# Optimization experiments

Measured on AMD Instinct MI355X. Metric: run time of the kernel, lower is better.

## Reference

```python
import jax, jax.numpy as jnp
import numpy as np

DIM, EMBED, HEADS = 768, 512, 8
HEAD_DIM = EMBED // HEADS


def setup_inputs() -> dict:
    key = jax.random.key(0)
    ks = jax.random.split(key, 11)
    B, S = 4, 2048
    s = 0.02
    return {
        "query": jax.random.normal(ks[0], (B, S, DIM), jnp.float32),
        "key": jax.random.normal(ks[1], (B, S, DIM), jnp.float32),
        "value": jax.random.normal(ks[2], (B, S, DIM), jnp.float32),
        "wq": jax.random.normal(ks[3], (DIM, EMBED), jnp.float32) * s,
        "bq": jnp.zeros((EMBED,), jnp.float32),
        "wk": jax.random.normal(ks[4], (DIM, EMBED), jnp.float32) * s,
        "bk": jnp.zeros((EMBED,), jnp.float32),
        "wv": jax.random.normal(ks[5], (DIM, EMBED), jnp.float32) * s,
        "bv": jnp.zeros((EMBED,), jnp.float32),
        "wo": jax.random.normal(ks[6], (EMBED, DIM), jnp.float32) * s,
        "bo": jnp.zeros((DIM,), jnp.float32),
    }


def reference(query, key, value, wq, bq, wk, bk, wv, bv, wo, bo):
    B, S, _ = query.shape
    # QKV projections -> [B, H, S, Dh]
    def split_heads(x):
        return x.reshape(B, -1, HEADS, HEAD_DIM).transpose(0, 2, 1, 3)
    q = split_heads(query @ wq + bq)
    k = split_heads(key @ wk + bk)
    v = split_heads(value @ wv + bv)
    scores = jnp.einsum("bhqd,bhkd->bhqk", q, k) / jnp.sqrt(jnp.float32(HEAD_DIM))
    p = jax.nn.softmax(scores, axis=-1)
    x = jnp.einsum("bhqk,bhkd->bhqd", p, v)
    x = x.transpose(0, 2, 1, 3).reshape(B, S, EMBED)
    return x @ wo + bo
```

## Files before the change

### kernel.cpp

```cpp
#include <hip/hip_runtime.h>
#include <math.h>

#define NH   8
#define HD   64
#define BS   4
#define SEQL 2048
#define DIMX 768
#define EMB  512
#define MROWS (BS*SEQL)
#define NSPLIT 2
#define KSPAN (SEQL/NSPLIT)

typedef __attribute__((ext_vector_type(4))) float          f32x4;
typedef __attribute__((ext_vector_type(8))) __bf16         bf16x8;
typedef __attribute__((ext_vector_type(8))) unsigned short u16x8;
typedef __attribute__((ext_vector_type(4))) unsigned short u16x4;

union BF8 { u16x8 u; bf16x8 b; };

__device__ __forceinline__ unsigned short f2bf(float x) {
    unsigned int u = __float_as_uint(x);
    u += 0x7FFFu + ((u >> 16) & 1u);
    return (unsigned short)(u >> 16);
}

#if __has_builtin(__builtin_amdgcn_exp2f)
#define EXP2F(x) __builtin_amdgcn_exp2f(x)
#else
#define EXP2F(x) exp2f(x)
#endif

__device__ __forceinline__ bf16x8 ldb8(const unsigned short* p) {
    return *(const bf16x8*)p;
}

__device__ __forceinline__ void gload16(const unsigned short* g, unsigned short* l) {
    __builtin_amdgcn_global_load_lds(
        (const __attribute__((address_space(1))) unsigned int*)(const void*)g,
        (__attribute__((address_space(3))) unsigned int*)(void*)l,
        16, 0, 0);
}

__global__ __launch_bounds__(256)
void transpose_w4(const float* __restrict__ w0, const float* __restrict__ w1,
                  const float* __restrict__ w2, const float* __restrict__ w3,
                  unsigned short* __restrict__ o0, unsigned short* __restrict__ o1,
                  unsigned short* __restrict__ o2, unsigned short* __restrict__ o3)
{
    __shared__ float sm[32][33];
    const int which = blockIdx.y;
    const float* in; unsigned short* out; int R, C;
    if      (which == 0) { in = w0; out = o0; R = DIMX; C = EMB;  }
    else if (which == 1) { in = w1; out = o1; R = DIMX; C = EMB;  }
    else if (which == 2) { in = w2; out = o2; R = DIMX; C = EMB;  }
    else                 { in = w3; out = o3; R = EMB;  C = DIMX; }
    const int nbx = C / 32;
    const int rB = (blockIdx.x / nbx) * 32, cB = (blockIdx.x % nbx) * 32;
    const int row = threadIdx.x >> 3, c4 = (threadIdx.x & 7) * 4;
    f32x4 v = *(const f32x4*)&in[(size_t)(rB + row) * C + cB + c4];
    sm[row][c4 + 0] = v[0]; sm[row][c4 + 1] = v[1];
    sm[row][c4 + 2] = v[2]; sm[row][c4 + 3] = v[3];
    __syncthreads();
    u16x4 o;
    o[0] = f2bf(sm[c4 + 0][row]); o[1] = f2bf(sm[c4 + 1][row]);
    o[2] = f2bf(sm[c4 + 2][row]); o[3] = f2bf(sm[c4 + 3][row]);
    *(u16x4*)&out[(size_t)(cB + row) * R + rB + c4] = o;
}

template<bool DIRECT, int AMODE>
__device__ __forceinline__ void gemm_core(
    const float* __restrict__ A, const float* __restrict__ A2,
    const float* __restrict__ lp0, const float* __restrict__ lp1,
    const unsigned short* __restrict__ Bt,
    int K, int lda, int mBase, int nBase,
    unsigned short* __restrict__ smA, unsigned short* __restrict__ smB,
    f32x4 (&acc)[4][4])
{
    const int tid = threadIdx.x;
    const int lane = tid & 63, w = tid >> 6;
    const int quad = lane >> 4, lanem = lane & 15;
    const int wm = w >> 1, wn = w & 1;
    const int r8 = lane >> 3, ch = lane & 7;
    const int swz = ((ch ^ r8) << 3);

    const f32x4 z4 = {0.f, 0.f, 0.f, 0.f};
    #pragma unroll
    for (int i = 0; i < 4; ++i)
        #pragma unroll
        for (int j = 0; j < 4; ++j) acc[i][j] = z4;

    const int fxor = (lanem & 7);

    for (int k0 = 0; k0 < K; k0 += 64) {
        u16x8 sa[4];
        #pragma unroll
        for (int j = 0; j < 4; ++j) {
            const int m = mBase + (w * 4 + j) * 8 + r8;
            const int kc = k0 + swz;
            if constexpr (AMODE == 1) {
                const float* ap = &A[(size_t)m * lda + kc];
                f32x4 x0 = *(const f32x4*)ap;
                f32x4 x1 = *(const f32x4*)(ap + 4);
                #pragma unroll
                for (int r = 0; r < 4; ++r) { sa[j][r] = f2bf(x0[r]); sa[j][4 + r] = f2bf(x1[r]); }
            } else {
                const int q = m & 2047, bb = m >> 11, hh = kc >> 6, dd = kc & 63;
                const size_t off = ((((size_t)((bb << 3) | hh)) * 2048 + q) << 6) + dd;
                f32x4 a0 = *(const f32x4*)&A [off];
                f32x4 a1 = *(const f32x4*)&A [off + 4];
                f32x4 c0 = *(const f32x4*)&A2[off];
                f32x4 c1 = *(const f32x4*)&A2[off + 4];
                const float rl = 1.f / (lp0[off >> 6] + lp1[off >> 6]);
                #pragma unroll
                for (int r = 0; r < 4; ++r) {
                    sa[j][r]     = f2bf((a0[r] + c0[r]) * rl);
                    sa[j][4 + r] = f2bf((a1[r] + c1[r]) * rl);
                }
            }
        }
        __syncthreads();
        #pragma unroll
        for (int j = 0; j < 4; ++j)
            *(u16x8*)&smA[(w * 4 + j) * 512 + lane * 8] = sa[j];
        #pragma unroll
        for (int j = 0; j < 4; ++j) {
            const int row = (w * 4 + j) * 8 + r8;
            gload16(&Bt[(size_t)(nBase + row) * K + k0 + swz], smB + (w * 4 + j) * 512);
        }
        __syncthreads();
        #pragma unroll
        for (int kk = 0; kk < 64; kk += 32) {
            const int cb = kk >> 3;
            bf16x8 xa[4], wb[4];
            #pragma unroll
            for (int mt = 0; mt < 4; ++mt)
                xa[mt] = ldb8(&smA[(wm * 64 + mt * 16 + lanem) * 64 + (((cb + quad) ^ fxor) << 3)]);
            #pragma unroll
            for (int nt = 0; nt < 4; ++nt)
                wb[nt] = ldb8(&smB[(wn * 64 + nt * 16 + lanem) * 64 + (((cb + quad) ^ fxor) << 3)]);
            if constexpr (DIRECT) {
                #pragma unroll
                for (int mt = 0; mt < 4; ++mt)
                    #pragma unroll
                    for (int nt = 0; nt < 4; ++nt)
                        acc[mt][nt] = __builtin_amdgcn_mfma_f32_16x16x32_bf16(xa[mt], wb[nt], acc[mt][nt], 0, 0, 0);
            } else {
                #pragma unroll
                for (int nt = 0; nt < 4; ++nt)
                    #pragma unroll
                    for (int mt = 0; mt < 4; ++mt)
                        acc[nt][mt] = __builtin_amdgcn_mfma_f32_16x16x32_bf16(wb[nt], xa[mt], acc[nt][mt], 0, 0, 0);
            }
        }
    }
}

__global__ __launch_bounds__(256)
void gemm_qkv(const float* __restrict__ Xq, const float* __restrict__ Xk,
              const float* __restrict__ Xv, const unsigned short* __restrict__ Wt,
              const float* __restrict__ bq, const float* __restrict__ bk,
              const float* __restrict__ bv,
              unsigned short* __restrict__ Qb, unsigned short* __restrict__ Kb,
              unsigned short* __restrict__ Vtb)
{
    __shared__ unsigned short smA[128 * 64];
    __shared__ unsigned short smB[128 * 64];
    const int id = blockIdx.x;
    const int xcd = id & 7, j = id >> 3;
    const int nIdx = j & 3, pr = j >> 2;
    const int p = pr * 8 + xcd;
    const int z = p >> 6;
    const int mBase = (p & 63) * 128, nBase = nIdx * 128;

    const float* A = z == 0 ? Xq : (z == 1 ? Xk : Xv);
    const unsigned short* Bt = Wt + (size_t)z * (EMB * DIMX);
    const float* bias = z == 0 ? bq : (z == 1 ? bk : bv);

    const int tid = threadIdx.x;
    const int lane = tid & 63, w = tid >> 6;
    const int quad = lane >> 4, lanem = lane & 15;
    const int wm = w >> 1, wn = w & 1;

    f32x4 acc[4][4];
    if (z == 2) {
        gemm_core<true, 1>(A, nullptr, nullptr, nullptr, Bt, DIMX, DIMX, mBase, nBase, smA, smB, acc);
        #pragma unroll
        for (int mt = 0; mt < 4; ++mt) {
            const int sg = mBase + wm * 64 + mt * 16 + quad * 4;
            const int b = sg >> 11, s = sg & 2047;
            #pragma unroll
            for (int nt = 0; nt < 4; ++nt) {
                const int de = nBase + wn * 64 + nt * 16 + lanem;
                const float bvv = bias[de];
                const int h = de >> 6, dh = de & 63;
                u16x4 ov;
                #pragma unroll
                for (int r = 0; r < 4; ++r) ov[r] = f2bf(acc[mt][nt][r] + bvv);
                *(u16x4*)&Vtb[((size_t)((b * NH + h) * HD + dh) << 11) + s] = ov;
            }
        }
    } else {
        gemm_core<false, 1>(A, nullptr, nullptr, nullptr, Bt, DIMX, DIMX, mBase, nBase, smA, smB, acc);
        const float os = (z == 0) ? 0.18033688f : 1.0f;
        unsigned short* C = (z == 0) ? Qb : Kb;
        #pragma unroll
        for (int nt = 0; nt < 4; ++nt) {
            const int n0 = nBase + wn * 64 + nt * 16 + quad * 4;
            const f32x4 b4 = *(const f32x4*)&bias[n0];
            #pragma unroll
            for (int mt = 0; mt < 4; ++mt) {
                const int m = mBase + wm * 64 + mt * 16 + lanem;
                u16x4 ov;
                #pragma unroll
                for (int r = 0; r < 4; ++r) ov[r] = f2bf((acc[nt][mt][r] + b4[r]) * os);
                *(u16x4*)&C[(size_t)m * EMB + n0] = ov;
            }
        }
    }
}

__global__ __launch_bounds__(256)
void gemm_out(const float* __restrict__ Opart, const float* __restrict__ lpart,
              const unsigned short* __restrict__ Wot,
              const float* __restrict__ bo, float* __restrict__ out)
{
    __shared__ unsigned short smA[128 * 64];
    __shared__ unsigned short smB[128 * 64];
    const int id = blockIdx.x;
    const int xcd = id & 7, j = id >> 3;
    const int nIdx = j % 6, pr = j / 6;
    const int mBase = (pr * 8 + xcd) * 128, nBase = nIdx * 128;
    const int tid = threadIdx.x;
    const int lane = tid & 63, w = tid >> 6;
    const int quad = lane >> 4, lanem = lane & 15;
    const int wm = w >> 1, wn = w & 1;

    const float* Op1 = Opart + (size_t)32 * SEQL * HD;
    const float* lp1 = lpart + (size_t)32 * SEQL;

    f32x4 acc[4][4];
    gemm_core<false, 2>(Opart, Op1, lpart, lp1, Wot, EMB, EMB, mBase, nBase, smA, smB, acc);
    #pragma unroll
    for (int nt = 0; nt < 4; ++nt) {
        const int n0 = nBase + wn * 64 + nt * 16 + quad * 4;
        const f32x4 b4 = *(const f32x4*)&bo[n0];
        #pragma unroll
        for (int mt = 0; mt < 4; ++mt) {
            const int m = mBase + wm * 64 + mt * 16 + lanem;
            f32x4 ov = acc[nt][mt] + b4;
            *(f32x4*)&out[(size_t)m * DIMX + n0] = ov;
        }
    }
}

__global__ __launch_bounds__(256)
void attn_mfma(const unsigned short* __restrict__ Qb, const unsigned short* __restrict__ Kb,
               const unsigned short* __restrict__ Vt,
               float* __restrict__ Opart, float* __restrict__ lpart)
{
    __shared__ unsigned short smK[64 * 72];
    __shared__ unsigned short smV[64 * 72];
    __shared__ unsigned short smP[4][32 * 72];
    const int id = blockIdx.x;
    const int bh = ((id & 7) << 2) | ((id >> 3) & 3);
    const int rest = id >> 5;
    const int qb = rest & 15, sp = rest >> 4;
    const int b = bh >> 3, h = bh & 7;

    const int tid = threadIdx.x;
    const int w = tid >> 6, lane = tid & 63;
    const int quad = lane >> 4, lanem = lane & 15;

    bf16x8 aq[2][2];
    #pragma unroll
    for (int rg = 0; rg < 2; ++rg) {
        const size_t qrow = (size_t)(b * SEQL + qb * 128 + w * 32 + rg * 16 + lanem) * EMB + h * HD;
        aq[rg][0] = ldb8(&Qb[qrow + quad * 8]);
        aq[rg][1] = ldb8(&Qb[qrow + 32 + quad * 8]);
    }

    const f32x4 z4 = {0.f, 0.f, 0.f, 0.f};
    f32x4 o[4][2];
    f32x4 ls[2] = {z4, z4};
    #pragma unroll
    for (int dt = 0; dt < 4; ++dt)
        #pragma unroll
        for (int rg = 0; rg < 2; ++rg) o[dt][rg] = z4;

    BF8 ones;
    #pragma unroll
    for (int i = 0; i < 8; ++i) ones.u[i] = 0x3F80;

    const unsigned short* Kbase = Kb + (size_t)b * SEQL * EMB + h * HD;
    const unsigned short* Vbase = Vt + (size_t)bh * HD * SEQL;
    unsigned short* pW = &smP[w][0];
    const int srow = tid >> 3, c8 = (tid & 7) * 8;

    for (int t = 0; t < KSPAN / 64; ++t) {
        const int k0 = sp * KSPAN + t * 64;
        u16x8 kv[2], vv[2];
        #pragma unroll
        for (int p = 0; p < 2; ++p) {
            kv[p] = *(const u16x8*)&Kbase[(size_t)(k0 + srow + p * 32) * EMB + c8];
            vv[p] = *(const u16x8*)&Vbase[(size_t)(srow + p * 32) * SEQL + k0 + c8];
        }
        __syncthreads();
        #pragma unroll
        for (int p = 0; p < 2; ++p) {
            *(u16x8*)&smK[(srow + p * 32) * 72 + c8] = kv[p];
            *(u16x8*)&smV[(srow + p * 32) * 72 + c8] = vv[p];
        }
        __syncthreads();

        #pragma unroll
        for (int nt = 0; nt < 4; ++nt) {
            bf16x8 bk0 = ldb8(&smK[(nt * 16 + lanem) * 72 + quad * 8]);
            bf16x8 bk1 = ldb8(&smK[(nt * 16 + lanem) * 72 + 32 + quad * 8]);
            #pragma unroll
            for (int rg = 0; rg < 2; ++rg) {
                f32x4 s = __builtin_amdgcn_mfma_f32_16x16x32_bf16(bk0, aq[rg][0], z4, 0, 0, 0);
                s = __builtin_amdgcn_mfma_f32_16x16x32_bf16(bk1, aq[rg][1], s, 0, 0, 0);
                u16x4 pk;
                #pragma unroll
                for (int r = 0; r < 4; ++r)
                    pk[r] = (unsigned short)(__float_as_uint(EXP2F(s[r])) >> 16);
                *(u16x4*)&pW[(rg * 16 + lanem) * 72 + nt * 16 + quad * 4] = pk;
            }
        }
        bf16x8 pb[2][2];
        #pragma unroll
        for (int rg = 0; rg < 2; ++rg) {
            pb[rg][0] = ldb8(&pW[(rg * 16 + lanem) * 72 + quad * 8]);
            pb[rg][1] = ldb8(&pW[(rg * 16 + lanem) * 72 + 32 + quad * 8]);
        }
        #pragma unroll
        for (int dt = 0; dt < 4; ++dt) {
            bf16x8 av0 = ldb8(&smV[(dt * 16 + lanem) * 72 + quad * 8]);
            bf16x8 av1 = ldb8(&smV[(dt * 16 + lanem) * 72 + 32 + quad * 8]);
            #pragma unroll
            for (int rg = 0; rg < 2; ++rg) {
                o[dt][rg] = __builtin_amdgcn_mfma_f32_16x16x32_bf16(av0, pb[rg][0], o[dt][rg], 0, 0, 0);
                o[dt][rg] = __builtin_amdgcn_mfma_f32_16x16x32_bf16(av1, pb[rg][1], o[dt][rg], 0, 0, 0);
            }
        }
        #pragma unroll
        for (int rg = 0; rg < 2; ++rg) {
            ls[rg] = __builtin_amdgcn_mfma_f32_16x16x32_bf16(ones.b, pb[rg][0], ls[rg], 0, 0, 0);
            ls[rg] = __builtin_amdgcn_mfma_f32_16x16x32_bf16(ones.b, pb[rg][1], ls[rg], 0, 0, 0);
        }
    }

    #pragma unroll
    for (int rg = 0; rg < 2; ++rg) {
        const int qloc = qb * 128 + w * 32 + rg * 16 + lanem;
        float* orow = Opart + ((size_t)sp * 32 * SEQL + (size_t)bh * SEQL + qloc) * HD;
        #pragma unroll
        for (int dt = 0; dt < 4; ++dt)
            *(f32x4*)&orow[dt * 16 + quad * 4] = o[dt][rg];
        if (quad == 0)
            lpart[(size_t)sp * 32 * SEQL + (size_t)bh * SEQL + qloc] = ls[rg][0];
    }
}

extern "C" void kernel_launch(void* const* d_in, const int* in_sizes, int n_in,
                              void* d_out, int out_size, void* d_ws, size_t ws_size,
                              hipStream_t stream) {
    (void)in_sizes; (void)n_in; (void)out_size; (void)ws_size;
    const float* query = (const float*)d_in[0];
    const float* key   = (const float*)d_in[1];
    const float* value = (const float*)d_in[2];
    const float* wq = (const float*)d_in[3];
    const float* bq = (const float*)d_in[4];
    const float* wk = (const float*)d_in[5];
    const float* bk = (const float*)d_in[6];
    const float* wv = (const float*)d_in[7];
    const float* bv = (const float*)d_in[8];
    const float* wo = (const float*)d_in[9];
    const float* bo = (const float*)d_in[10];
    float* out = (float*)d_out;

    char* ws = (char*)d_ws;
    float*          Opart = (float*)(ws);
    float*          lpart = (float*)(ws + 33554432);
    unsigned short* Wt    = (unsigned short*)(ws + 37748736);
    unsigned short* Wot   = (unsigned short*)(ws + 40108032);
    unsigned short* Qbuf  = (unsigned short*)(ws + 40894464);
    unsigned short* Kbuf  = (unsigned short*)(ws + 49283072);
    unsigned short* Vtb   = (unsigned short*)(ws + 57671680);

    const dim3 blk(256);

    transpose_w4<<<dim3(384, 4), blk, 0, stream>>>(wq, wk, wv, wo,
        Wt, Wt + (size_t)EMB * DIMX, Wt + 2 * (size_t)EMB * DIMX, Wot);

    gemm_qkv<<<dim3(768), blk, 0, stream>>>(
        query, key, value, Wt, bq, bk, bv, Qbuf, Kbuf, Vtb);

    attn_mfma<<<dim3(32 * 16 * NSPLIT), blk, 0, stream>>>(Qbuf, Kbuf, Vtb, Opart, lpart);

    gemm_out<<<dim3(384), blk, 0, stream>>>(Opart, lpart, Wot, bo, out);
}
```

Baseline: 238.1 us.

## Double-buffer shared-memory tiles in GEMM core to overlap loads with MFMA

The GEMM core now keeps two shared-memory buffers for A and B. The next K-step's global loads (and the async B copy) are issued before the MFMA work on the current buffer, and the bf16 conversion and store of A into the other buffer happens after the compute. This removes one barrier per step and hides global-load latency behind the matrix work. In exchange, shared memory per block doubles to 64KB and register pressure rises from the prefetch registers, which may reduce occupancy.

```diff
diff --git a/kernel.cpp b/kernel.cpp
--- a/kernel.cpp
+++ b/kernel.cpp
@@ -82,6 +82,7 @@
     const int wm = w >> 1, wn = w & 1;
     const int r8 = lane >> 3, ch = lane & 7;
     const int swz = ((ch ^ r8) << 3);
+    const int fxor = (lanem & 7);
 
     const f32x4 z4 = {0.f, 0.f, 0.f, 0.f};
     #pragma unroll
@@ -89,55 +90,82 @@
         #pragma unroll
         for (int j = 0; j < 4; ++j) acc[i][j] = z4;
 
-    const int fxor = (lanem & 7);
-
-    for (int k0 = 0; k0 < K; k0 += 64) {
-        u16x8 sa[4];
-        #pragma unroll
-        for (int j = 0; j < 4; ++j) {
-            const int m = mBase + (w * 4 + j) * 8 + r8;
-            const int kc = k0 + swz;
-            if constexpr (AMODE == 1) {
-                const float* ap = &A[(size_t)m * lda + kc];
-                f32x4 x0 = *(const f32x4*)ap;
-                f32x4 x1 = *(const f32x4*)(ap + 4);
-                #pragma unroll
-                for (int r = 0; r < 4; ++r) { sa[j][r] = f2bf(x0[r]); sa[j][4 + r] = f2bf(x1[r]); }
-            } else {
-                const int q = m & 2047, bb = m >> 11, hh = kc >> 6, dd = kc & 63;
-                const size_t off = ((((size_t)((bb << 3) | hh)) * 2048 + q) << 6) + dd;
-                f32x4 a0 = *(const f32x4*)&A [off];
-                f32x4 a1 = *(const f32x4*)&A [off + 4];
-                f32x4 c0 = *(const f32x4*)&A2[off];
-                f32x4 c1 = *(const f32x4*)&A2[off + 4];
-                const float rl = 1.f / (lp0[off >> 6] + lp1[off >> 6]);
-                #pragma unroll
-                for (int r = 0; r < 4; ++r) {
-                    sa[j][r]     = f2bf((a0[r] + c0[r]) * rl);
-                    sa[j][4 + r] = f2bf((a1[r] + c1[r]) * rl);
+    const int nsteps = K / 64;
+
+    #pragma unroll
+    for (int j = 0; j < 4; ++j) {
+        const int row = (w * 4 + j) * 8 + r8;
+        const int m = mBase + row;
+        u16x8 sa;
+        if constexpr (AMODE == 1) {
+            const float* ap = &A[(size_t)m * lda + swz];
+            f32x4 x0 = *(const f32x4*)ap;
+            f32x4 x1 = *(const f32x4*)(ap + 4);
+            #pragma unroll
+            for (int r = 0; r < 4; ++r) { sa[r] = f2bf(x0[r]); sa[4 + r] = f2bf(x1[r]); }
+        } else {
+            const int q = m & 2047, bb = m >> 11, hh = swz >> 6, dd = swz & 63;
+            const size_t off = ((((size_t)((bb << 3) | hh)) * 2048 + q) << 6) + dd;
+            f32x4 a0 = *(const f32x4*)&A [off];
+            f32x4 a1 = *(const f32x4*)&A [off + 4];
+            f32x4 c0 = *(const f32x4*)&A2[off];
+            f32x4 c1 = *(const f32x4*)&A2[off + 4];
+            const float rl = 1.f / (lp0[off >> 6] + lp1[off >> 6]);
+            #pragma unroll
+            for (int r = 0; r < 4; ++r) {
+                sa[r]     = f2bf((a0[r] + c0[r]) * rl);
+                sa[4 + r] = f2bf((a1[r] + c1[r]) * rl);
+            }
+        }
+        *(u16x8*)&smA[(w * 4 + j) * 512 + lane * 8] = sa;
+        gload16(&Bt[(size_t)(nBase + row) * K + swz], smB + (w * 4 + j) * 512);
+    }
+    __syncthreads();
+
+    int cur = 0;
+    for (int t = 0; t < nsteps; ++t) {
+        const int nxt = cur ^ 1;
+        const int k1 = (t + 1) * 64;
+        const bool more = (t + 1) < nsteps;
+
+        f32x4 px0[4], px1[4], pc0[4], pc1[4];
+        float pls[4];
+        if (more) {
+            #pragma unroll
+            for (int j = 0; j < 4; ++j) {
+                const int row = (w * 4 + j) * 8 + r8;
+                const int m = mBase + row;
+                const int kc = k1 + swz;
+                if constexpr (AMODE == 1) {
+                    const float* ap = &A[(size_t)m * lda + kc];
+                    px0[j] = *(const f32x4*)ap;
+                    px1[j] = *(const f32x4*)(ap + 4);
+                } else {
+                    const int q = m & 2047, bb = m >> 11, hh = kc >> 6, dd = kc & 63;
+                    const size_t off = ((((size_t)((bb << 3) | hh)) * 2048 + q) << 6) + dd;
+                    px0[j] = *(const f32x4*)&A [off];
+                    px1[j] = *(const f32x4*)&A [off + 4];
+                    pc0[j] = *(const f32x4*)&A2[off];
+                    pc1[j] = *(const f32x4*)&A2[off + 4];
+                    pls[j] = lp0[off >> 6] + lp1[off >> 6];
                 }
-            }
-        }
-        __syncthreads();
-        #pragma unroll
-        for (int j = 0; j < 4; ++j)
-            *(u16x8*)&smA[(w * 4 + j) * 512 + lane * 8] = sa[j];
-        #pragma unroll
-        for (int j = 0; j < 4; ++j) {
-            const int row = (w * 4 + j) * 8 + r8;
-            gload16(&Bt[(size_t)(nBase + row) * K + k0 + swz], smB + (w * 4 + j) * 512);
-        }
-        __syncthreads();
+                gload16(&Bt[(size_t)(nBase + row) * K + k1 + swz],
+                        smB + nxt * 8192 + (w * 4 + j) * 512);
+            }
+        }
+
+        const unsigned short* sA = smA + cur * 8192;
+        const unsigned short* sB = smB + cur * 8192;
         #pragma unroll
         for (int kk = 0; kk < 64; kk += 32) {
             const int cb = kk >> 3;
             bf16x8 xa[4], wb[4];
             #pragma unroll
             for (int mt = 0; mt < 4; ++mt)
-                xa[mt] = ldb8(&smA[(wm * 64 + mt * 16 + lanem) * 64 + (((cb + quad) ^ fxor) << 3)]);
+                xa[mt] = ldb8(&sA[(wm * 64 + mt * 16 + lanem) * 64 + (((cb + quad) ^ fxor) << 3)]);
             #pragma unroll
             for (int nt = 0; nt < 4; ++nt)
-                wb[nt] = ldb8(&smB[(wn * 64 + nt * 16 + lanem) * 64 + (((cb + quad) ^ fxor) << 3)]);
+                wb[nt] = ldb8(&sB[(wn * 64 + nt * 16 + lanem) * 64 + (((cb + quad) ^ fxor) << 3)]);
             if constexpr (DIRECT) {
                 #pragma unroll
                 for (int mt = 0; mt < 4; ++mt)
@@ -152,6 +180,27 @@
                         acc[nt][mt] = __builtin_amdgcn_mfma_f32_16x16x32_bf16(wb[nt], xa[mt], acc[nt][mt], 0, 0, 0);
             }
         }
+
+        if (more) {
+            #pragma unroll
+            for (int j = 0; j < 4; ++j) {
+                u16x8 sa;
+                if constexpr (AMODE == 1) {
+                    #pragma unroll
+                    for (int r = 0; r < 4; ++r) { sa[r] = f2bf(px0[j][r]); sa[4 + r] = f2bf(px1[j][r]); }
+                } else {
+                    const float rl = 1.f / pls[j];
+                    #pragma unroll
+                    for (int r = 0; r < 4; ++r) {
+                        sa[r]     = f2bf((px0[j][r] + pc0[j][r]) * rl);
+                        sa[4 + r] = f2bf((px1[j][r] + pc1[j][r]) * rl);
+                    }
+                }
+                *(u16x8*)&smA[nxt * 8192 + (w * 4 + j) * 512 + lane * 8] = sa;
+            }
+        }
+        __syncthreads();
+        cur = nxt;
     }
 }
 
@@ -163,8 +212,8 @@
               unsigned short* __restrict__ Qb, unsigned short* __restrict__ Kb,
               unsigned short* __restrict__ Vtb)
 {
-    __shared__ unsigned short smA[128 * 64];
-    __shared__ unsigned short smB[128 * 64];
+    __shared__ unsigned short smA[2 * 128 * 64];
+    __shared__ unsigned short smB[2 * 128 * 64];
     const int id = blockIdx.x;
     const int xcd = id & 7, j = id >> 3;
     const int nIdx = j & 3, pr = j >> 2;
@@ -224,8 +273,8 @@
               const unsigned short* __restrict__ Wot,
               const float* __restrict__ bo, float* __restrict__ out)
 {
-    __shared__ unsigned short smA[128 * 64];
-    __shared__ unsigned short smB[128 * 64];
+    __shared__ unsigned short smA[2 * 128 * 64];
+    __shared__ unsigned short smB[2 * 128 * 64];
     const int id = blockIdx.x;
     const int xcd = id & 7, j = id >> 3;
     const int nIdx = j % 6, pr = j / 6;
```

After: 260.8 us. 9.6% more time.
